# Kernel optimization log

Measured on AMD Instinct MI355X. Metric: run time of the kernel, lower is better.

## Reference

```python
import jax, jax.numpy as jnp
import numpy as np

# Production-scale dims
B, DZ, NW, NH, K = 8, 32, 48, 48, 25          # batch, dim_z, grid width/height, n_objects_max
W_RAW = H_RAW = 384.0                          # raw image size
SIZE_MIN, SIZE_MAX = 12.0, 48.0                # object size bounds
SCORE_T, OVER_T = 0.1, 0.3                     # score_threshold, overlap_threshold


def _conv1x1(x, w, b):
    # x: (B, d, nW, nH), w: (o, d), b: (o,) -> (B, o, nW, nH)  [Decoder1by1Linear]
    return jnp.einsum('bdwh,od->bowh', x, w) + b[None, :, None, None]


def _to_box_list(x):
    # (B, nW, nH) -> (N, B) with N = nW*nH, matching convert_to_box_list's permute(2,3,0,1).view
    return jnp.transpose(x, (1, 2, 0)).reshape(-1, x.shape[0])


def _nms(probT, x1, y1, x2, y2, k_max, score_t, over_t):
    # probT, x1..y2: (B, N). Greedy score/overlap NMS -> idx (B, K) int32, mask (B, N) float
    area = (x2 - x1) * (y2 - y1)
    xi1 = jnp.maximum(x1[:, :, None], x1[:, None, :])
    yi1 = jnp.maximum(y1[:, :, None], y1[:, None, :])
    xi2 = jnp.minimum(x2[:, :, None], x2[:, None, :])
    yi2 = jnp.minimum(y2[:, :, None], y2[:, None, :])
    inter = jnp.clip(xi2 - xi1, 0.0) * jnp.clip(yi2 - yi1, 0.0)
    union = area[:, :, None] + area[:, None, :] - inter
    iou = inter / jnp.maximum(union, 1e-8)                      # (B, N, N)
    possible0 = probT > score_t
    Bsz, N = probT.shape
    idx0 = jnp.zeros((Bsz, k_max), jnp.int32)
    val0 = jnp.zeros((Bsz, k_max), bool)

    def body(k, carry):
        possible, idxb, valb = carry
        masked = jnp.where(possible, probT, -jnp.inf)
        sel = jnp.argmax(masked, axis=1).astype(jnp.int32)      # (B,)
        ok = jnp.take_along_axis(possible, sel[:, None], axis=1)[:, 0]
        row = jnp.take_along_axis(iou, sel[:, None, None], axis=1)[:, 0, :]
        possible = possible & (row <= over_t)                   # suppresses sel itself (IoU=1)
        return possible, idxb.at[:, k].set(sel), valb.at[:, k].set(ok)

    _, idxb, valb = jax.lax.fori_loop(0, k_max, body, (possible0, idx0, val0))
    mask = jnp.zeros((Bsz, N), probT.dtype).at[jnp.arange(Bsz)[:, None], idxb].max(
        valb.astype(probT.dtype))
    return idxb, mask


def setup_inputs() -> dict:
    key = jax.random.key(0)
    ks = jax.random.split(key, 5)
    return {
        'zwhere_sample': jax.random.normal(ks[0], (B, DZ, NW, NH), jnp.float32),
        'w_zwhere': 0.2 * jax.random.normal(ks[1], (4, DZ), jnp.float32),
        'b_zwhere': jnp.zeros((4,), jnp.float32),
        'logit_sample': jax.random.normal(ks[2], (B, DZ, NW, NH), jnp.float32),
        'w_logit': 0.2 * jax.random.normal(ks[3], (1, DZ), jnp.float32),
        'b_logit': jnp.zeros((1,), jnp.float32),
        'weight_logits': jax.random.normal(ks[4], (K, B, 1, int(W_RAW), int(H_RAW)), jnp.float32),
    }


def reference(zwhere_sample, w_zwhere, b_zwhere, logit_sample, w_logit, b_logit, weight_logits):
    nW, nH = zwhere_sample.shape[-2:]
    # --- box decoding from zwhere latent map ---
    t = jax.nn.sigmoid(_conv1x1(zwhere_sample, w_zwhere, b_zwhere))  # (B,4,nW,nH)
    tx, ty, tw, th = t[:, 0], t[:, 1], t[:, 2], t[:, 3]
    ix = jnp.arange(nW, dtype=t.dtype)[:, None]   # ij meshgrid rows
    iy = jnp.arange(nH, dtype=t.dtype)[None, :]
    bx = W_RAW * (ix + tx) / nW
    by = H_RAW * (iy + ty) / nH
    bw = SIZE_MIN + (SIZE_MAX - SIZE_MIN) * tw
    bh = SIZE_MIN + (SIZE_MAX - SIZE_MIN) * th
    bx_l, by_l = _to_box_list(bx), _to_box_list(by)   # (N, B)
    bw_l, bh_l = _to_box_list(bw), _to_box_list(bh)
    # --- probability map from logit latent map ---
    p_map = jax.nn.sigmoid(_conv1x1(logit_sample, w_logit, b_logit))  # (B,1,nW,nH)
    prob_all = _to_box_list(p_map[:, 0])              # (N, B)
    probT = prob_all.T                                 # (B, N)
    x1 = (bx_l - 0.5 * bw_l).T
    x2 = (bx_l + 0.5 * bw_l).T
    y1 = (by_l - 0.5 * bh_l).T
    y2 = (by_l + 0.5 * bh_l).T
    # --- NMS under stop_gradient (torch.no_grad in original) ---
    sg = jax.lax.stop_gradient
    idxb, maskB = _nms(sg(probT), sg(x1), sg(y1), sg(x2), sg(y2), K, SCORE_T, OVER_T)
    # prob_few = gather(prob_all * nms_mask, index_top_k): differentiable w.r.t. prob_all
    prob_few = jnp.take_along_axis(probT * maskB, idxb, axis=1).T   # (K, B)
    # --- mask compositing (from_weights_to_masks over the object dim) ---
    big_weight = jax.nn.softplus(weight_logits)       # (K, B, 1, W, H)
    sum_w = jnp.sum(big_weight, axis=0, keepdims=True)
    big_mask = jnp.tanh(sum_w) * (big_weight / jnp.clip(sum_w, 1e-6))
    # probability-weighted masks (downstream compositing)
    return prob_few[:, :, None, None, None] * big_mask  # (K, B, 1, W, H)
```

## Files before the change

kernel.cpp:

```cpp
#include <hip/hip_runtime.h>
#include <math.h>

#define BATCH 8
#define DZ    32
#define NWH   48
#define NBOX  (NWH*NWH)
#define KMAX  25
#define PIX   (384*384)
#define NTHR  576
#define NW9   9

typedef float vfloat4 __attribute__((ext_vector_type(4)));

__device__ __forceinline__ float sigm(float x) { return 1.0f / (1.0f + expf(-x)); }
__device__ __forceinline__ float sp_fast(float x) {
    return fmaxf(x, 0.0f) + __logf(1.0f + __expf(-fabsf(x)));
}

__global__ __launch_bounds__(NTHR) void boxnms_kernel(
    const float* __restrict__ z, const float* __restrict__ wz, const float* __restrict__ bz,
    const float* __restrict__ lg, const float* __restrict__ wl, const float* __restrict__ bl,
    float* __restrict__ pfT)
{
    __shared__ vfloat4 boxS[NBOX];
    __shared__ float   prS[NBOX];
    __shared__ unsigned long long keyB[2][NW9];
    __shared__ int idxA[KMAX], okA[KMAX];

    const int b = blockIdx.x, t = threadIdx.x;
    const int iw = t / 12, ihq = t % 12;

    const float* zb = z  + (((size_t)b * DZ) * NWH + iw) * NWH + ihq * 4;
    const float* lb = lg + (((size_t)b * DZ) * NWH + iw) * NWH + ihq * 4;
    float b0 = bz[0], b1 = bz[1], b2 = bz[2], b3 = bz[3], blg = bl[0];
    vfloat4 a0 = {b0,b0,b0,b0}, a1 = {b1,b1,b1,b1}, a2 = {b2,b2,b2,b2},
            a3 = {b3,b3,b3,b3}, al = {blg,blg,blg,blg};
    #pragma unroll 8
    for (int d = 0; d < DZ; ++d) {
        vfloat4 zv = *(const vfloat4*)(zb + (size_t)d * NBOX);
        vfloat4 lv = *(const vfloat4*)(lb + (size_t)d * NBOX);
        float w0 = wz[d], w1 = wz[32+d], w2 = wz[64+d], w3 = wz[96+d], wv = wl[d];
        a0 += zv * w0; a1 += zv * w1; a2 += zv * w2; a3 += zv * w3; al += lv * wv;
    }

    float x1r[4], y1r[4], x2r[4], y2r[4], arr[4], mkv[4];
    int   nbs[4];
    {
        float t0v[4] = {a0.x,a0.y,a0.z,a0.w};
        float t1v[4] = {a1.x,a1.y,a1.z,a1.w};
        float t2v[4] = {a2.x,a2.y,a2.z,a2.w};
        float t3v[4] = {a3.x,a3.y,a3.z,a3.w};
        float alv[4] = {al.x,al.y,al.z,al.w};
        #pragma unroll
        for (int c = 0; c < 4; ++c) {
            float tx = sigm(t0v[c]), ty = sigm(t1v[c]), tw = sigm(t2v[c]), th = sigm(t3v[c]);
            float bx = 8.0f * ((float)iw + tx);
            float by = 8.0f * ((float)(ihq*4 + c) + ty);
            float bw = 12.0f + 36.0f * tw;
            float bh = 12.0f + 36.0f * th;
            float x1 = bx - 0.5f*bw, y1 = by - 0.5f*bh, x2 = bx + 0.5f*bw, y2 = by + 0.5f*bh;
            float p  = sigm(alv[c]);
            int   n  = iw * NWH + ihq*4 + c;
            x1r[c]=x1; y1r[c]=y1; x2r[c]=x2; y2r[c]=y2;
            arr[c] = (x2-x1)*(y2-y1);
            mkv[c] = (p > 0.1f) ? p : -INFINITY;
            nbs[c] = n;
            boxS[n] = (vfloat4){x1,y1,x2,y2};
            prS[n]  = p;
        }
    }

    float sx1=0.f, sy1=0.f, sx2=0.f, sy2=0.f, sar=0.f;
    for (int k = 0; k < KMAX; ++k) {
        unsigned long long best = 0ULL;
        #pragma unroll
        for (int c = 0; c < 4; ++c) {
            if (k > 0 && mkv[c] != -INFINITY) {
                float xi1 = fmaxf(sx1, x1r[c]);
                float yi1 = fmaxf(sy1, y1r[c]);
                float xi2 = fminf(sx2, x2r[c]);
                float yi2 = fminf(sy2, y2r[c]);
                float inter = fmaxf(xi2 - xi1, 0.f) * fmaxf(yi2 - yi1, 0.f);
                float uni   = sar + arr[c] - inter;
                float iou   = inter / fmaxf(uni, 1e-8f);
                if (iou > 0.3f) mkv[c] = -INFINITY;
            }
            if (mkv[c] != -INFINITY) {
                unsigned long long kk =
                    ((unsigned long long)__float_as_uint(mkv[c]) << 32) | (unsigned int)(~nbs[c]);
                if (kk > best) best = kk;
            }
        }
        #pragma unroll
        for (int off = 32; off > 0; off >>= 1) {
            unsigned long long o = __shfl_down(best, off);
            if (o > best) best = o;
        }
        if ((t & 63) == 0) keyB[k & 1][t >> 6] = best;
        __syncthreads();
        unsigned long long m = keyB[k & 1][0];
        #pragma unroll
        for (int w = 1; w < NW9; ++w) {
            unsigned long long o = keyB[k & 1][w];
            if (o > m) m = o;
        }
        int sel = (m == 0ULL) ? 0 : (int)(~(unsigned int)(m & 0xFFFFFFFFULL));
        if (t == 0) { idxA[k] = sel; okA[k] = (m != 0ULL); }
        vfloat4 sb = boxS[sel];
        sx1 = sb.x; sy1 = sb.y; sx2 = sb.z; sy2 = sb.w;
        sar = (sx2 - sx1) * (sy2 - sy1);
    }

    if (t == 0) {
        #pragma unroll 1
        for (int k = 0; k < KMAX; ++k) {
            float mm = 0.f;
            for (int k2 = 0; k2 < KMAX; ++k2)
                if (idxA[k2] == idxA[k] && okA[k2]) mm = 1.f;
            pfT[b * 32 + k] = prS[idxA[k]] * mm;
        }
    }
}

__global__ __launch_bounds__(256) void big_kernel(const float* __restrict__ wlg,
                                                  const float* __restrict__ pfT,
                                                  float* __restrict__ out)
{
    const size_t stride = (size_t)BATCH * PIX;
    const int t = threadIdx.x;
    const int r = t & 3;
    const size_t j = ((size_t)blockIdx.x * 64 + (t >> 2)) * 4;
    const int b = (int)(blockIdx.x / 576);
    const int kb = 6 * r;
    const float* base = wlg + (size_t)kb * stride + j;

    vfloat4 acc = {0.f, 0.f, 0.f, 0.f};
    vfloat4 sp0, sp1, sp2, sp3, sp4, sp5;
#define LOADSP(s) { vfloat4 v = *(const vfloat4*)(base + (size_t)(s) * stride); \
    sp##s = (vfloat4){ sp_fast(v.x), sp_fast(v.y), sp_fast(v.z), sp_fast(v.w) }; \
    acc += sp##s; }
    LOADSP(0) LOADSP(1) LOADSP(2) LOADSP(3) LOADSP(4) LOADSP(5)
#undef LOADSP
    vfloat4 sp6 = {0.f, 0.f, 0.f, 0.f};
    if (r == 0) {
        vfloat4 v = *(const vfloat4*)(wlg + (size_t)24 * stride + j);
        sp6 = (vfloat4){ sp_fast(v.x), sp_fast(v.y), sp_fast(v.z), sp_fast(v.w) };
        acc += sp6;
    }

    #pragma unroll
    for (int mlane = 1; mlane <= 2; mlane <<= 1) {
        acc.x += __shfl_xor(acc.x, mlane);
        acc.y += __shfl_xor(acc.y, mlane);
        acc.z += __shfl_xor(acc.z, mlane);
        acc.w += __shfl_xor(acc.w, mlane);
    }

    vfloat4 m;
    {
        float ex = __expf(-2.f*acc.x), ey = __expf(-2.f*acc.y),
              ez = __expf(-2.f*acc.z), ew = __expf(-2.f*acc.w);
        m.x = (1.f - ex) * __builtin_amdgcn_rcpf(1.f + ex) * __builtin_amdgcn_rcpf(fmaxf(acc.x, 1e-6f));
        m.y = (1.f - ey) * __builtin_amdgcn_rcpf(1.f + ey) * __builtin_amdgcn_rcpf(fmaxf(acc.y, 1e-6f));
        m.z = (1.f - ez) * __builtin_amdgcn_rcpf(1.f + ez) * __builtin_amdgcn_rcpf(fmaxf(acc.z, 1e-6f));
        m.w = (1.f - ew) * __builtin_amdgcn_rcpf(1.f + ew) * __builtin_amdgcn_rcpf(fmaxf(acc.w, 1e-6f));
    }

    const float* pfb = pfT + b * 32 + kb;
    float* ob = out + (size_t)kb * stride + j;
#define STORE(s) { float c = pfb[s]; \
    vfloat4 o = { c * m.x * sp##s.x, c * m.y * sp##s.y, c * m.z * sp##s.z, c * m.w * sp##s.w }; \
    __builtin_nontemporal_store(o, (vfloat4*)(ob + (size_t)(s) * stride)); }
    STORE(0) STORE(1) STORE(2) STORE(3) STORE(4) STORE(5)
#undef STORE
    if (r == 0) {
        float c = pfT[b * 32 + 24];
        vfloat4 o = { c * m.x * sp6.x, c * m.y * sp6.y, c * m.z * sp6.z, c * m.w * sp6.w };
        __builtin_nontemporal_store(o, (vfloat4*)(out + (size_t)24 * stride + j));
    }
}

extern "C" void kernel_launch(void* const* d_in, const int* in_sizes, int n_in,
                              void* d_out, int out_size, void* d_ws, size_t ws_size,
                              hipStream_t stream)
{
    const float* zwhere = (const float*)d_in[0];
    const float* w_zw   = (const float*)d_in[1];
    const float* b_zw   = (const float*)d_in[2];
    const float* logit  = (const float*)d_in[3];
    const float* w_lg   = (const float*)d_in[4];
    const float* b_lg   = (const float*)d_in[5];
    const float* wlogit = (const float*)d_in[6];
    float* out = (float*)d_out;
    float* pfT = (float*)d_ws;

    boxnms_kernel<<<BATCH, NTHR, 0, stream>>>(zwhere, w_zw, b_zw, logit, w_lg, b_lg, pfT);
    big_kernel<<<(BATCH * PIX) / 256, 256, 0, stream>>>(wlogit, pfT, out);
}
```

Baseline: 94.28 us.

## Split conv out of NMS kernel and software-pipeline chunked big kernel

The 1x1 convolution that produces boxes and probabilities moves out of the 8-block NMS kernel into its own kernel spread over 18 blocks, so the expensive global reads use more CUs. Box data reaches the NMS kernel through workspace buffers. The compositing kernel now handles four chunks per thread and double-buffers the loads of the next chunk, with four times fewer blocks. The cost is an extra launch plus a round trip through the workspace, and higher register use in the big kernel.

```diff
diff --git a/kernel.cpp b/kernel.cpp
--- a/kernel.cpp
+++ b/kernel.cpp
@@ -7,8 +7,9 @@
 #define NBOX  (NWH*NWH)
 #define KMAX  25
 #define PIX   (384*384)
-#define NTHR  576
+#define NTOT  (BATCH*NBOX)
 #define NW9   9
+#define CHUNKS 4
 
 typedef float vfloat4 __attribute__((ext_vector_type(4)));
 
@@ -17,18 +18,14 @@
     return fmaxf(x, 0.0f) + __logf(1.0f + __expf(-fabsf(x)));
 }
 
-__global__ __launch_bounds__(NTHR) void boxnms_kernel(
+__global__ __launch_bounds__(256) void conv_kernel(
     const float* __restrict__ z, const float* __restrict__ wz, const float* __restrict__ bz,
     const float* __restrict__ lg, const float* __restrict__ wl, const float* __restrict__ bl,
-    float* __restrict__ pfT)
-{
-    __shared__ vfloat4 boxS[NBOX];
-    __shared__ float   prS[NBOX];
-    __shared__ unsigned long long keyB[2][NW9];
-    __shared__ int idxA[KMAX], okA[KMAX];
-
-    const int b = blockIdx.x, t = threadIdx.x;
-    const int iw = t / 12, ihq = t % 12;
+    float* __restrict__ ws)
+{
+    int t = blockIdx.x * 256 + threadIdx.x;
+    int b = t / 576, j = t % 576;
+    int iw = j / 12, ihq = j % 12;
 
     const float* zb = z  + (((size_t)b * DZ) * NWH + iw) * NWH + ihq * 4;
     const float* lb = lg + (((size_t)b * DZ) * NWH + iw) * NWH + ihq * 4;
@@ -43,32 +40,63 @@
         a0 += zv * w0; a1 += zv * w1; a2 += zv * w2; a3 += zv * w3; al += lv * wv;
     }
 
-    float x1r[4], y1r[4], x2r[4], y2r[4], arr[4], mkv[4];
-    int   nbs[4];
-    {
-        float t0v[4] = {a0.x,a0.y,a0.z,a0.w};
-        float t1v[4] = {a1.x,a1.y,a1.z,a1.w};
-        float t2v[4] = {a2.x,a2.y,a2.z,a2.w};
-        float t3v[4] = {a3.x,a3.y,a3.z,a3.w};
-        float alv[4] = {al.x,al.y,al.z,al.w};
-        #pragma unroll
-        for (int c = 0; c < 4; ++c) {
-            float tx = sigm(t0v[c]), ty = sigm(t1v[c]), tw = sigm(t2v[c]), th = sigm(t3v[c]);
-            float bx = 8.0f * ((float)iw + tx);
-            float by = 8.0f * ((float)(ihq*4 + c) + ty);
-            float bw = 12.0f + 36.0f * tw;
-            float bh = 12.0f + 36.0f * th;
-            float x1 = bx - 0.5f*bw, y1 = by - 0.5f*bh, x2 = bx + 0.5f*bw, y2 = by + 0.5f*bh;
-            float p  = sigm(alv[c]);
-            int   n  = iw * NWH + ihq*4 + c;
-            x1r[c]=x1; y1r[c]=y1; x2r[c]=x2; y2r[c]=y2;
-            arr[c] = (x2-x1)*(y2-y1);
-            mkv[c] = (p > 0.1f) ? p : -INFINITY;
-            nbs[c] = n;
-            boxS[n] = (vfloat4){x1,y1,x2,y2};
-            prS[n]  = p;
-        }
-    }
+    float t0v[4] = {a0.x,a0.y,a0.z,a0.w};
+    float t1v[4] = {a1.x,a1.y,a1.z,a1.w};
+    float t2v[4] = {a2.x,a2.y,a2.z,a2.w};
+    float t3v[4] = {a3.x,a3.y,a3.z,a3.w};
+    float alv[4] = {al.x,al.y,al.z,al.w};
+    float x1o[4], y1o[4], x2o[4], y2o[4], po[4];
+    #pragma unroll
+    for (int c = 0; c < 4; ++c) {
+        float tx = sigm(t0v[c]), ty = sigm(t1v[c]), tw = sigm(t2v[c]), th = sigm(t3v[c]);
+        float bx = 8.0f * ((float)iw + tx);
+        float by = 8.0f * ((float)(ihq*4 + c) + ty);
+        float bw = 12.0f + 36.0f * tw;
+        float bh = 12.0f + 36.0f * th;
+        x1o[c] = bx - 0.5f*bw;  y1o[c] = by - 0.5f*bh;
+        x2o[c] = bx + 0.5f*bw;  y2o[c] = by + 0.5f*bh;
+        po[c]  = sigm(alv[c]);
+    }
+    int o = b * NBOX + iw * NWH + ihq * 4;
+    *(vfloat4*)(ws + 0*NTOT + o) = (vfloat4){x1o[0],x1o[1],x1o[2],x1o[3]};
+    *(vfloat4*)(ws + 1*NTOT + o) = (vfloat4){y1o[0],y1o[1],y1o[2],y1o[3]};
+    *(vfloat4*)(ws + 2*NTOT + o) = (vfloat4){x2o[0],x2o[1],x2o[2],x2o[3]};
+    *(vfloat4*)(ws + 3*NTOT + o) = (vfloat4){y2o[0],y2o[1],y2o[2],y2o[3]};
+    *(vfloat4*)(ws + 4*NTOT + o) = (vfloat4){po[0], po[1], po[2], po[3]};
+}
+
+__global__ __launch_bounds__(576) void nms_kernel(const float* __restrict__ ws,
+                                                  float* __restrict__ pfT)
+{
+    __shared__ vfloat4 boxS[NBOX];
+    __shared__ float   prS[NBOX];
+    __shared__ unsigned long long keyB[2][NW9];
+    __shared__ int idxA[KMAX], okA[KMAX];
+
+    const int b = blockIdx.x, t = threadIdx.x;
+    const int n0 = t * 4;
+    const int o  = b * NBOX + n0;
+
+    vfloat4 X1 = *(const vfloat4*)(ws + 0*NTOT + o);
+    vfloat4 Y1 = *(const vfloat4*)(ws + 1*NTOT + o);
+    vfloat4 X2 = *(const vfloat4*)(ws + 2*NTOT + o);
+    vfloat4 Y2 = *(const vfloat4*)(ws + 3*NTOT + o);
+    vfloat4 P  = *(const vfloat4*)(ws + 4*NTOT + o);
+
+    float x1r[4] = {X1.x,X1.y,X1.z,X1.w};
+    float y1r[4] = {Y1.x,Y1.y,Y1.z,Y1.w};
+    float x2r[4] = {X2.x,X2.y,X2.z,X2.w};
+    float y2r[4] = {Y2.x,Y2.y,Y2.z,Y2.w};
+    float pv [4] = {P.x, P.y, P.z, P.w};
+    float arr[4], mkv[4];
+    #pragma unroll
+    for (int c = 0; c < 4; ++c) {
+        arr[c] = (x2r[c]-x1r[c]) * (y2r[c]-y1r[c]);
+        mkv[c] = (pv[c] > 0.1f) ? pv[c] : -INFINITY;
+        boxS[n0+c] = (vfloat4){x1r[c], y1r[c], x2r[c], y2r[c]};
+        prS [n0+c] = pv[c];
+    }
+    __syncthreads();
 
     float sx1=0.f, sy1=0.f, sx2=0.f, sy2=0.f, sar=0.f;
     for (int k = 0; k < KMAX; ++k) {
@@ -87,22 +115,22 @@
             }
             if (mkv[c] != -INFINITY) {
                 unsigned long long kk =
-                    ((unsigned long long)__float_as_uint(mkv[c]) << 32) | (unsigned int)(~nbs[c]);
+                    ((unsigned long long)__float_as_uint(mkv[c]) << 32) | (unsigned int)(~(n0+c));
                 if (kk > best) best = kk;
             }
         }
         #pragma unroll
         for (int off = 32; off > 0; off >>= 1) {
-            unsigned long long o = __shfl_down(best, off);
-            if (o > best) best = o;
+            unsigned long long o2 = __shfl_down(best, off);
+            if (o2 > best) best = o2;
         }
         if ((t & 63) == 0) keyB[k & 1][t >> 6] = best;
         __syncthreads();
         unsigned long long m = keyB[k & 1][0];
         #pragma unroll
         for (int w = 1; w < NW9; ++w) {
-            unsigned long long o = keyB[k & 1][w];
-            if (o > m) m = o;
+            unsigned long long o2 = keyB[k & 1][w];
+            if (o2 > m) m = o2;
         }
         int sel = (m == 0ULL) ? 0 : (int)(~(unsigned int)(m & 0xFFFFFFFFULL));
         if (t == 0) { idxA[k] = sel; okA[k] = (m != 0ULL); }
@@ -129,54 +157,79 @@
     const size_t stride = (size_t)BATCH * PIX;
     const int t = threadIdx.x;
     const int r = t & 3;
-    const size_t j = ((size_t)blockIdx.x * 64 + (t >> 2)) * 4;
-    const int b = (int)(blockIdx.x / 576);
     const int kb = 6 * r;
-    const float* base = wlg + (size_t)kb * stride + j;
-
-    vfloat4 acc = {0.f, 0.f, 0.f, 0.f};
-    vfloat4 sp0, sp1, sp2, sp3, sp4, sp5;
-#define LOADSP(s) { vfloat4 v = *(const vfloat4*)(base + (size_t)(s) * stride); \
-    sp##s = (vfloat4){ sp_fast(v.x), sp_fast(v.y), sp_fast(v.z), sp_fast(v.w) }; \
-    acc += sp##s; }
-    LOADSP(0) LOADSP(1) LOADSP(2) LOADSP(3) LOADSP(4) LOADSP(5)
-#undef LOADSP
-    vfloat4 sp6 = {0.f, 0.f, 0.f, 0.f};
-    if (r == 0) {
-        vfloat4 v = *(const vfloat4*)(wlg + (size_t)24 * stride + j);
-        sp6 = (vfloat4){ sp_fast(v.x), sp_fast(v.y), sp_fast(v.z), sp_fast(v.w) };
-        acc += sp6;
-    }
-
-    #pragma unroll
-    for (int mlane = 1; mlane <= 2; mlane <<= 1) {
-        acc.x += __shfl_xor(acc.x, mlane);
-        acc.y += __shfl_xor(acc.y, mlane);
-        acc.z += __shfl_xor(acc.z, mlane);
-        acc.w += __shfl_xor(acc.w, mlane);
-    }
-
-    vfloat4 m;
-    {
-        float ex = __expf(-2.f*acc.x), ey = __expf(-2.f*acc.y),
-              ez = __expf(-2.f*acc.z), ew = __expf(-2.f*acc.w);
-        m.x = (1.f - ex) * __builtin_amdgcn_rcpf(1.f + ex) * __builtin_amdgcn_rcpf(fmaxf(acc.x, 1e-6f));
-        m.y = (1.f - ey) * __builtin_amdgcn_rcpf(1.f + ey) * __builtin_amdgcn_rcpf(fmaxf(acc.y, 1e-6f));
-        m.z = (1.f - ez) * __builtin_amdgcn_rcpf(1.f + ez) * __builtin_amdgcn_rcpf(fmaxf(acc.z, 1e-6f));
-        m.w = (1.f - ew) * __builtin_amdgcn_rcpf(1.f + ew) * __builtin_amdgcn_rcpf(fmaxf(acc.w, 1e-6f));
-    }
-
-    const float* pfb = pfT + b * 32 + kb;
-    float* ob = out + (size_t)kb * stride + j;
-#define STORE(s) { float c = pfb[s]; \
-    vfloat4 o = { c * m.x * sp##s.x, c * m.y * sp##s.y, c * m.z * sp##s.z, c * m.w * sp##s.w }; \
-    __builtin_nontemporal_store(o, (vfloat4*)(ob + (size_t)(s) * stride)); }
-    STORE(0) STORE(1) STORE(2) STORE(3) STORE(4) STORE(5)
-#undef STORE
-    if (r == 0) {
-        float c = pfT[b * 32 + 24];
-        vfloat4 o = { c * m.x * sp6.x, c * m.y * sp6.y, c * m.z * sp6.z, c * m.w * sp6.w };
-        __builtin_nontemporal_store(o, (vfloat4*)(out + (size_t)24 * stride + j));
+    const int b = blockIdx.x / 144;
+    const size_t j0 = ((size_t)blockIdx.x * 256 + (t >> 2)) * 4;
+    const float* pbase = wlg + (size_t)kb * stride;
+    const float* p24   = wlg + (size_t)24 * stride;
+
+    float pfv[7];
+    #pragma unroll
+    for (int s = 0; s < 6; ++s) pfv[s] = pfT[b * 32 + kb + s];
+    pfv[6] = pfT[b * 32 + 24];
+
+    vfloat4 buf[2][7];
+    #pragma unroll
+    for (int s = 0; s < 6; ++s) buf[0][s] = *(const vfloat4*)(pbase + (size_t)s * stride + j0);
+    if (r == 0) buf[0][6] = *(const vfloat4*)(p24 + j0);
+
+    #pragma unroll
+    for (int i = 0; i < CHUNKS; ++i) {
+        const size_t j = j0 + (size_t)i * 256;
+        if (i + 1 < CHUNKS) {
+            const size_t jn = j + 256;
+            #pragma unroll
+            for (int s = 0; s < 6; ++s)
+                buf[(i+1)&1][s] = *(const vfloat4*)(pbase + (size_t)s * stride + jn);
+            if (r == 0) buf[(i+1)&1][6] = *(const vfloat4*)(p24 + jn);
+        }
+
+        vfloat4 acc = {0.f, 0.f, 0.f, 0.f};
+        #pragma unroll
+        for (int s = 0; s < 6; ++s) {
+            vfloat4 v = buf[i&1][s];
+            vfloat4 sv = { sp_fast(v.x), sp_fast(v.y), sp_fast(v.z), sp_fast(v.w) };
+            buf[i&1][s] = sv;
+            acc += sv;
+        }
+        vfloat4 sv6 = {0.f, 0.f, 0.f, 0.f};
+        if (r == 0) {
+            vfloat4 v = buf[i&1][6];
+            sv6 = (vfloat4){ sp_fast(v.x), sp_fast(v.y), sp_fast(v.z), sp_fast(v.w) };
+        }
+        acc += sv6;
+
+        #pragma unroll
+        for (int mlane = 1; mlane <= 2; mlane <<= 1) {
+            acc.x += __shfl_xor(acc.x, mlane);
+            acc.y += __shfl_xor(acc.y, mlane);
+            acc.z += __shfl_xor(acc.z, mlane);
+            acc.w += __shfl_xor(acc.w, mlane);
+        }
+
+        vfloat4 m;
+        {
+            float ex = __expf(-2.f*acc.x), ey = __expf(-2.f*acc.y),
+                  ez = __expf(-2.f*acc.z), ew = __expf(-2.f*acc.w);
+            m.x = (1.f - ex) * __builtin_amdgcn_rcpf(1.f + ex) * __builtin_amdgcn_rcpf(fmaxf(acc.x, 1e-6f));
+            m.y = (1.f - ey) * __builtin_amdgcn_rcpf(1.f + ey) * __builtin_amdgcn_rcpf(fmaxf(acc.y, 1e-6f));
+            m.z = (1.f - ez) * __builtin_amdgcn_rcpf(1.f + ez) * __builtin_amdgcn_rcpf(fmaxf(acc.z, 1e-6f));
+            m.w = (1.f - ew) * __builtin_amdgcn_rcpf(1.f + ew) * __builtin_amdgcn_rcpf(fmaxf(acc.w, 1e-6f));
+        }
+
+        float* ob = out + (size_t)kb * stride + j;
+        #pragma unroll
+        for (int s = 0; s < 6; ++s) {
+            float c = pfv[s];
+            vfloat4 sv = buf[i&1][s];
+            vfloat4 o = { c * m.x * sv.x, c * m.y * sv.y, c * m.z * sv.z, c * m.w * sv.w };
+            __builtin_nontemporal_store(o, (vfloat4*)(ob + (size_t)s * stride));
+        }
+        if (r == 0) {
+            float c = pfv[6];
+            vfloat4 o = { c * m.x * sv6.x, c * m.y * sv6.y, c * m.z * sv6.z, c * m.w * sv6.w };
+            __builtin_nontemporal_store(o, (vfloat4*)(out + (size_t)24 * stride + j));
+        }
     }
 }
 
@@ -192,8 +245,10 @@
     const float* b_lg   = (const float*)d_in[5];
     const float* wlogit = (const float*)d_in[6];
     float* out = (float*)d_out;
-    float* pfT = (float*)d_ws;
-
-    boxnms_kernel<<<BATCH, NTHR, 0, stream>>>(zwhere, w_zw, b_zw, logit, w_lg, b_lg, pfT);
-    big_kernel<<<(BATCH * PIX) / 256, 256, 0, stream>>>(wlogit, pfT, out);
-}
+    float* ws  = (float*)d_ws;
+    float* pfT = ws + 5 * NTOT;
+
+    conv_kernel<<<(BATCH*576)/256, 256, 0, stream>>>(zwhere, w_zw, b_zw, logit, w_lg, b_lg, ws);
+    nms_kernel<<<BATCH, 576, 0, stream>>>(ws, pfT);
+    big_kernel<<<(BATCH*PIX)/1024, 256, 0, stream>>>(wlogit, pfT, out);
+}
```

Measured after the change: 99.47 us. 5.5% more time.

## Split box conv out of NMS kernel into a wide grid kernel; drop nontemporal stores

Applied to the files above, without the earlier changes.

Moves the 1x1 conv, sigmoid and box computation out of the 8-block NMS kernel into a separate kernel with 72 blocks of 64 threads, so the input reads spread over many CUs instead of 8. Box corners and probabilities go through a workspace buffer to the NMS kernel, which loads them and runs the same greedy loop. It adds a kernel launch and a global round trip. The big kernel also switches from nontemporal stores to plain stores.

```diff
diff --git a/kernel.cpp b/kernel.cpp
--- a/kernel.cpp
+++ b/kernel.cpp
@@ -7,7 +7,7 @@
 #define NBOX  (NWH*NWH)
 #define KMAX  25
 #define PIX   (384*384)
-#define NTHR  576
+#define NTOT  (BATCH*NBOX)
 #define NW9   9
 
 typedef float vfloat4 __attribute__((ext_vector_type(4)));
@@ -17,18 +17,14 @@
     return fmaxf(x, 0.0f) + __logf(1.0f + __expf(-fabsf(x)));
 }
 
-__global__ __launch_bounds__(NTHR) void boxnms_kernel(
+__global__ __launch_bounds__(64) void conv_kernel(
     const float* __restrict__ z, const float* __restrict__ wz, const float* __restrict__ bz,
     const float* __restrict__ lg, const float* __restrict__ wl, const float* __restrict__ bl,
-    float* __restrict__ pfT)
-{
-    __shared__ vfloat4 boxS[NBOX];
-    __shared__ float   prS[NBOX];
-    __shared__ unsigned long long keyB[2][NW9];
-    __shared__ int idxA[KMAX], okA[KMAX];
-
-    const int b = blockIdx.x, t = threadIdx.x;
-    const int iw = t / 12, ihq = t % 12;
+    float* __restrict__ ws)
+{
+    int t = blockIdx.x * 64 + threadIdx.x;
+    int b = t / 576, j = t % 576;
+    int iw = j / 12, ihq = j % 12;
 
     const float* zb = z  + (((size_t)b * DZ) * NWH + iw) * NWH + ihq * 4;
     const float* lb = lg + (((size_t)b * DZ) * NWH + iw) * NWH + ihq * 4;
@@ -43,32 +39,63 @@
         a0 += zv * w0; a1 += zv * w1; a2 += zv * w2; a3 += zv * w3; al += lv * wv;
     }
 
-    float x1r[4], y1r[4], x2r[4], y2r[4], arr[4], mkv[4];
-    int   nbs[4];
-    {
-        float t0v[4] = {a0.x,a0.y,a0.z,a0.w};
-        float t1v[4] = {a1.x,a1.y,a1.z,a1.w};
-        float t2v[4] = {a2.x,a2.y,a2.z,a2.w};
-        float t3v[4] = {a3.x,a3.y,a3.z,a3.w};
-        float alv[4] = {al.x,al.y,al.z,al.w};
-        #pragma unroll
-        for (int c = 0; c < 4; ++c) {
-            float tx = sigm(t0v[c]), ty = sigm(t1v[c]), tw = sigm(t2v[c]), th = sigm(t3v[c]);
-            float bx = 8.0f * ((float)iw + tx);
-            float by = 8.0f * ((float)(ihq*4 + c) + ty);
-            float bw = 12.0f + 36.0f * tw;
-            float bh = 12.0f + 36.0f * th;
-            float x1 = bx - 0.5f*bw, y1 = by - 0.5f*bh, x2 = bx + 0.5f*bw, y2 = by + 0.5f*bh;
-            float p  = sigm(alv[c]);
-            int   n  = iw * NWH + ihq*4 + c;
-            x1r[c]=x1; y1r[c]=y1; x2r[c]=x2; y2r[c]=y2;
-            arr[c] = (x2-x1)*(y2-y1);
-            mkv[c] = (p > 0.1f) ? p : -INFINITY;
-            nbs[c] = n;
-            boxS[n] = (vfloat4){x1,y1,x2,y2};
-            prS[n]  = p;
-        }
-    }
+    float t0v[4] = {a0.x,a0.y,a0.z,a0.w};
+    float t1v[4] = {a1.x,a1.y,a1.z,a1.w};
+    float t2v[4] = {a2.x,a2.y,a2.z,a2.w};
+    float t3v[4] = {a3.x,a3.y,a3.z,a3.w};
+    float alv[4] = {al.x,al.y,al.z,al.w};
+    float x1o[4], y1o[4], x2o[4], y2o[4], po[4];
+    #pragma unroll
+    for (int c = 0; c < 4; ++c) {
+        float tx = sigm(t0v[c]), ty = sigm(t1v[c]), tw = sigm(t2v[c]), th = sigm(t3v[c]);
+        float bx = 8.0f * ((float)iw + tx);
+        float by = 8.0f * ((float)(ihq*4 + c) + ty);
+        float bw = 12.0f + 36.0f * tw;
+        float bh = 12.0f + 36.0f * th;
+        x1o[c] = bx - 0.5f*bw;  y1o[c] = by - 0.5f*bh;
+        x2o[c] = bx + 0.5f*bw;  y2o[c] = by + 0.5f*bh;
+        po[c]  = sigm(alv[c]);
+    }
+    int o = b * NBOX + iw * NWH + ihq * 4;
+    *(vfloat4*)(ws + 0*NTOT + o) = (vfloat4){x1o[0],x1o[1],x1o[2],x1o[3]};
+    *(vfloat4*)(ws + 1*NTOT + o) = (vfloat4){y1o[0],y1o[1],y1o[2],y1o[3]};
+    *(vfloat4*)(ws + 2*NTOT + o) = (vfloat4){x2o[0],x2o[1],x2o[2],x2o[3]};
+    *(vfloat4*)(ws + 3*NTOT + o) = (vfloat4){y2o[0],y2o[1],y2o[2],y2o[3]};
+    *(vfloat4*)(ws + 4*NTOT + o) = (vfloat4){po[0], po[1], po[2], po[3]};
+}
+
+__global__ __launch_bounds__(576) void nms_kernel(const float* __restrict__ ws,
+                                                  float* __restrict__ pfT)
+{
+    __shared__ vfloat4 boxS[NBOX];
+    __shared__ float   prS[NBOX];
+    __shared__ unsigned long long keyB[2][NW9];
+    __shared__ int idxA[KMAX], okA[KMAX];
+
+    const int b = blockIdx.x, t = threadIdx.x;
+    const int n0 = t * 4;
+    const int o  = b * NBOX + n0;
+
+    vfloat4 X1 = *(const vfloat4*)(ws + 0*NTOT + o);
+    vfloat4 Y1 = *(const vfloat4*)(ws + 1*NTOT + o);
+    vfloat4 X2 = *(const vfloat4*)(ws + 2*NTOT + o);
+    vfloat4 Y2 = *(const vfloat4*)(ws + 3*NTOT + o);
+    vfloat4 P  = *(const vfloat4*)(ws + 4*NTOT + o);
+
+    float x1r[4] = {X1.x,X1.y,X1.z,X1.w};
+    float y1r[4] = {Y1.x,Y1.y,Y1.z,Y1.w};
+    float x2r[4] = {X2.x,X2.y,X2.z,X2.w};
+    float y2r[4] = {Y2.x,Y2.y,Y2.z,Y2.w};
+    float pv [4] = {P.x, P.y, P.z, P.w};
+    float arr[4], mkv[4];
+    #pragma unroll
+    for (int c = 0; c < 4; ++c) {
+        arr[c] = (x2r[c]-x1r[c]) * (y2r[c]-y1r[c]);
+        mkv[c] = (pv[c] > 0.1f) ? pv[c] : -INFINITY;
+        boxS[n0+c] = (vfloat4){x1r[c], y1r[c], x2r[c], y2r[c]};
+        prS [n0+c] = pv[c];
+    }
+    __syncthreads();
 
     float sx1=0.f, sy1=0.f, sx2=0.f, sy2=0.f, sar=0.f;
     for (int k = 0; k < KMAX; ++k) {
@@ -87,22 +114,22 @@
             }
             if (mkv[c] != -INFINITY) {
                 unsigned long long kk =
-                    ((unsigned long long)__float_as_uint(mkv[c]) << 32) | (unsigned int)(~nbs[c]);
+                    ((unsigned long long)__float_as_uint(mkv[c]) << 32) | (unsigned int)(~(n0+c));
                 if (kk > best) best = kk;
             }
         }
         #pragma unroll
         for (int off = 32; off > 0; off >>= 1) {
-            unsigned long long o = __shfl_down(best, off);
-            if (o > best) best = o;
+            unsigned long long o2 = __shfl_down(best, off);
+            if (o2 > best) best = o2;
         }
         if ((t & 63) == 0) keyB[k & 1][t >> 6] = best;
         __syncthreads();
         unsigned long long m = keyB[k & 1][0];
         #pragma unroll
         for (int w = 1; w < NW9; ++w) {
-            unsigned long long o = keyB[k & 1][w];
-            if (o > m) m = o;
+            unsigned long long o2 = keyB[k & 1][w];
+            if (o2 > m) m = o2;
         }
         int sel = (m == 0ULL) ? 0 : (int)(~(unsigned int)(m & 0xFFFFFFFFULL));
         if (t == 0) { idxA[k] = sel; okA[k] = (m != 0ULL); }
@@ -170,13 +197,13 @@
     float* ob = out + (size_t)kb * stride + j;
 #define STORE(s) { float c = pfb[s]; \
     vfloat4 o = { c * m.x * sp##s.x, c * m.y * sp##s.y, c * m.z * sp##s.z, c * m.w * sp##s.w }; \
-    __builtin_nontemporal_store(o, (vfloat4*)(ob + (size_t)(s) * stride)); }
+    *(vfloat4*)(ob + (size_t)(s) * stride) = o; }
     STORE(0) STORE(1) STORE(2) STORE(3) STORE(4) STORE(5)
 #undef STORE
     if (r == 0) {
         float c = pfT[b * 32 + 24];
         vfloat4 o = { c * m.x * sp6.x, c * m.y * sp6.y, c * m.z * sp6.z, c * m.w * sp6.w };
-        __builtin_nontemporal_store(o, (vfloat4*)(out + (size_t)24 * stride + j));
+        *(vfloat4*)(out + (size_t)24 * stride + j) = o;
     }
 }
 
@@ -192,8 +219,10 @@
     const float* b_lg   = (const float*)d_in[5];
     const float* wlogit = (const float*)d_in[6];
     float* out = (float*)d_out;
-    float* pfT = (float*)d_ws;
-
-    boxnms_kernel<<<BATCH, NTHR, 0, stream>>>(zwhere, w_zw, b_zw, logit, w_lg, b_lg, pfT);
+    float* ws  = (float*)d_ws;
+    float* pfT = ws + 5 * NTOT;
+
+    conv_kernel<<<(BATCH*576)/64, 64, 0, stream>>>(zwhere, w_zw, b_zw, logit, w_lg, b_lg, ws);
+    nms_kernel<<<BATCH, 576, 0, stream>>>(ws, pfT);
     big_kernel<<<(BATCH * PIX) / 256, 256, 0, stream>>>(wlogit, pfT, out);
 }
```

After: 97.50 us. 3.4% more time.
